# Kernel tuning notes

Measured on AMD Instinct MI355X. Metric: run time of the kernel, lower is better.

## Reference

```python
import jax, jax.numpy as jnp
import numpy as np
import math

B, T, D = 2, 2048, 1024
NH = 16
HD = D // NH


def setup_inputs() -> dict:
    key = jax.random.key(0)
    k1, k2, k3 = jax.random.split(key, 3)
    scale = 0.02
    x = jax.random.normal(k1, (B, T, D), dtype=jnp.float32)
    Wqkv = jax.random.normal(k2, (D, 3 * D), dtype=jnp.float32) * scale
    bqkv = jnp.zeros((3 * D,), dtype=jnp.float32)
    Wproj = jax.random.normal(k3, (D, D), dtype=jnp.float32) * scale
    bproj = jnp.zeros((D,), dtype=jnp.float32)
    return {"x": x, "Wqkv": Wqkv, "bqkv": bqkv, "Wproj": Wproj, "bproj": bproj}


def reference(x, Wqkv, bqkv, Wproj, bproj):
    b, t, c = x.shape
    qkv = x @ Wqkv + bqkv                      # [B,T,3D]
    q, k, v = jnp.split(qkv, 3, axis=2)
    # [B,T,NH,HD] -> [B,NH,T,HD]
    q = q.reshape(b, t, NH, HD).transpose(0, 2, 1, 3)
    k = k.reshape(b, t, NH, HD).transpose(0, 2, 1, 3)
    v = v.reshape(b, t, NH, HD).transpose(0, 2, 1, 3)
    att = jnp.einsum('bhqd,bhkd->bhqk', q, k) / math.sqrt(HD)  # [B,NH,T,T]
    causal = jnp.tril(jnp.ones((t, t), dtype=bool))
    att = jnp.where(causal, att, -jnp.inf)
    att = jax.nn.softmax(att, axis=-1)
    y = jnp.einsum('bhqk,bhkd->bhqd', att, v)  # [B,NH,T,HD]
    y = y.transpose(0, 2, 1, 3).reshape(b, t, c)
    return y @ Wproj + bproj
```

## Files before the change

kernel.cpp:

```cpp
#include <hip/hip_runtime.h>
#include <hip/hip_bf16.h>

#define B_   2
#define T_   2048
#define D_   1024
#define NH_  16
#define HD_  64
#define MROWS (B_*T_)
#define HEADELEMS (B_*NH_*T_*HD_)

#define QSCALE 0.180336880f

typedef unsigned short u16;
typedef unsigned int   u32;

typedef float f32x4  __attribute__((ext_vector_type(4)));
typedef short bf16x8 __attribute__((ext_vector_type(8)));

#define GLP(g, l) __builtin_amdgcn_global_load_lds(                         \
    (const __attribute__((address_space(1))) void*)(g),                     \
    (__attribute__((address_space(3))) void*)(l), 16, 0, 0)

struct Fc { static constexpr bool value = false; };
struct Tc { static constexpr bool value = true;  };

__device__ __forceinline__ u16 f2bf(float f) {
    u32 x = __float_as_uint(f);
    u32 r = (x + 0x7fffu + ((x >> 16) & 1u)) >> 16;
    return (u16)r;
}
__device__ __forceinline__ u32 pkbf2(float a, float b) {
    __hip_bfloat162 h = __float22bfloat162_rn(make_float2(a, b));
    union { __hip_bfloat162 h2; u32 u; } cv; cv.h2 = h; return cv.u;
}

__device__ __forceinline__ void transpose_tile(const float* in, u16* out,
                                               int K, int N, int bx, int by,
                                               int t, float (*Ts)[65])
{
    const int n0 = bx * 64;
    const int k0 = by * 64;
    #pragma unroll
    for (int pass = 0; pass < 4; pass++) {
        const int r = pass * 16 + (t >> 4);
        const int c = (t & 15) * 4;
        float4 v = *(const float4*)(in + (size_t)(k0 + r) * N + n0 + c);
        Ts[r][c] = v.x; Ts[r][c+1] = v.y; Ts[r][c+2] = v.z; Ts[r][c+3] = v.w;
    }
    __syncthreads();
    #pragma unroll
    for (int pass = 0; pass < 2; pass++) {
        const int nn = pass * 32 + (t >> 3);
        const int kk = (t & 7) * 8;
        u16 o[8];
        #pragma unroll
        for (int j = 0; j < 8; j++) o[j] = f2bf(Ts[kk + j][nn]);
        *(uint4*)(out + (size_t)(n0 + nn) * K + k0 + kk) = *(const uint4*)o;
    }
}

__global__ __launch_bounds__(256)
void prep_kernel(const float* __restrict__ x, const float* __restrict__ Wqkv,
                 const float* __restrict__ Wproj, u16* __restrict__ xb,
                 u16* __restrict__ WqkvT, u16* __restrict__ WprojT)
{
    __shared__ float Ts[64][65];
    const int bid = blockIdx.x;
    const int t   = threadIdx.x;
    if (bid < 4096) {
        int i = bid * 256 + t;
        float4 v = ((const float4*)x)[i];
        ushort4 o;
        o.x = f2bf(v.x); o.y = f2bf(v.y); o.z = f2bf(v.z); o.w = f2bf(v.w);
        ((ushort4*)xb)[i] = o;
    } else if (bid < 4096 + 768) {
        int tb = bid - 4096;
        transpose_tile(Wqkv, WqkvT, D_, 3*D_, tb % 48, tb / 48, t, Ts);
    } else {
        int tb = bid - 4864;
        transpose_tile(Wproj, WprojT, D_, D_, tb % 16, tb / 16, t, Ts);
    }
}

__global__ __launch_bounds__(256)
void transpose_conv_kernel(const float* __restrict__ in, u16* __restrict__ out,
                           int K, int N)
{
    __shared__ float Ts[64][65];
    transpose_tile(in, out, K, N, blockIdx.x, blockIdx.y, threadIdx.x, Ts);
}

template <int MODE>
__global__ __launch_bounds__(256)
void gemm_mfma(const u16* __restrict__ A, const u16* __restrict__ BT,
               const float* __restrict__ bias, void* __restrict__ outv,
               int M, int N, int K)
{
    __shared__ u16 As[2][128][64];
    __shared__ u16 Bs[2][128][64];

    const int t    = threadIdx.x;
    const int wave = t >> 6;
    const int lane = t & 63;
    const int l16  = lane & 15;
    const int quad = lane >> 4;

    const int m0 = blockIdx.y * 128;
    const int n0 = blockIdx.x * 128;
    const int mb = (wave >> 1) * 64;
    const int nb = (wave & 1) * 64;

    const int srow = t >> 3;
    const int sseg = ((t & 7) ^ (srow & 7)) * 8;
    const int rw8  = wave * 8;

    const u16* gA = A  + (size_t)(m0 + srow) * K + sseg;
    const u16* gB = BT + (size_t)(n0 + srow) * K + sseg;

    const int fragcol = (quad ^ (l16 & 7)) * 8;

    f32x4 acc[4][4];
    #pragma unroll
    for (int i = 0; i < 4; i++)
        #pragma unroll
        for (int j = 0; j < 4; j++) acc[i][j] = (f32x4){0,0,0,0};

    auto STAGE = [&](int buf, int k0) {
        GLP(gA + k0,          &As[buf][rw8     ][0]);
        GLP(gA + k0 + 32*K,   &As[buf][rw8 + 32][0]);
        GLP(gA + k0 + 64*K,   &As[buf][rw8 + 64][0]);
        GLP(gA + k0 + 96*K,   &As[buf][rw8 + 96][0]);
        GLP(gB + k0,          &Bs[buf][rw8     ][0]);
        GLP(gB + k0 + 32*K,   &Bs[buf][rw8 + 32][0]);
        GLP(gB + k0 + 64*K,   &Bs[buf][rw8 + 64][0]);
        GLP(gB + k0 + 96*K,   &Bs[buf][rw8 + 96][0]);
    };

    const int nk = K >> 6;

    STAGE(0, 0);
    asm volatile("s_waitcnt vmcnt(0)" ::: "memory");
    __builtin_amdgcn_s_barrier();

    for (int kt = 0; kt < nk; ++kt) {
        const int cur = kt & 1;
        const bool have_next = (kt + 1 < nk);

        if (have_next) {
            STAGE(cur ^ 1, (kt + 1) << 6);
            asm volatile("s_waitcnt vmcnt(8)" ::: "memory");
        } else {
            asm volatile("s_waitcnt vmcnt(0)" ::: "memory");
        }
        __builtin_amdgcn_s_barrier();

        #pragma unroll
        for (int kk = 0; kk < 2; kk++) {
            const int fc = fragcol ^ (kk << 5);
            bf16x8 af[4], bfr[4];
            #pragma unroll
            for (int i = 0; i < 4; i++)
                af[i] = *(const bf16x8*)&As[cur][mb + i*16 + l16][fc];
            #pragma unroll
            for (int j = 0; j < 4; j++)
                bfr[j] = *(const bf16x8*)&Bs[cur][nb + j*16 + l16][fc];

            #pragma unroll
            for (int i = 0; i < 4; i++)
                #pragma unroll
                for (int j = 0; j < 4; j++)
                    acc[i][j] = __builtin_amdgcn_mfma_f32_16x16x32_bf16(
                        af[i], bfr[j], acc[i][j], 0, 0, 0);
        }

        if (have_next) {
            asm volatile("s_waitcnt lgkmcnt(0)" ::: "memory");
            __builtin_amdgcn_s_barrier();
        }
    }

    if (MODE == 0) {
        #pragma unroll
        for (int j = 0; j < 4; j++) {
            const int n = n0 + nb + j*16 + l16;
            const float bv = bias[n];
            #pragma unroll
            for (int i = 0; i < 4; i++) {
                #pragma unroll
                for (int r = 0; r < 4; r++) {
                    const int m = m0 + mb + i*16 + quad*4 + r;
                    ((float*)outv)[(size_t)m * N + n] = acc[i][j][r] + bv;
                }
            }
        }
    } else {
        const int sec = n0 >> 10;
        const int b   = m0 >> 11;
        const int tb  = m0 & 2047;
        if (sec < 2) {
            const float qs = (sec == 0) ? QSCALE : 1.f;
            #pragma unroll
            for (int j = 0; j < 4; j++) {
                const int n  = n0 + nb + j*16 + l16;
                const float bv = bias[n];
                const int dd = n & 1023;
                const int h  = dd >> 6;
                const int hd = dd & 63;
                u16* op = (u16*)outv + (size_t)sec * HEADELEMS
                        + ((size_t)(b*NH_ + h)) * T_ * HD_ + hd;
                #pragma unroll
                for (int i = 0; i < 4; i++) {
                    #pragma unroll
                    for (int r = 0; r < 4; r++) {
                        const int tt = tb + mb + i*16 + quad*4 + r;
                        op[(size_t)tt * HD_] = f2bf((acc[i][j][r] + bv) * qs);
                    }
                }
            }
        } else {
            #pragma unroll
            for (int j = 0; j < 4; j++) {
                const int n  = n0 + nb + j*16 + l16;
                const float bv = bias[n];
                const int dd = n & 1023;
                const int h  = dd >> 6;
                const int hd = dd & 63;
                u16* vp = (u16*)outv + (size_t)2 * HEADELEMS
                        + ((size_t)(b*NH_ + h)) * T_ * HD_
                        + (size_t)hd * T_ + tb + mb;
                #pragma unroll
                for (int i = 0; i < 4; i++) {
                    u16 o[4];
                    #pragma unroll
                    for (int r = 0; r < 4; r++) o[r] = f2bf(acc[i][j][r] + bv);
                    *(uint2*)(vp + i*16 + quad*4) = *(const uint2*)o;
                }
            }
        }
    }
}

__global__ __launch_bounds__(256)
void attn_mfma_kernel(const u16* __restrict__ Q, const u16* __restrict__ K,
                      const u16* __restrict__ VT, u16* __restrict__ y1)
{
    __shared__ u16 Ks[2][64][64];
    __shared__ u16 Vs[2][64][64];

    const int t    = threadIdx.x;
    const int wave = t >> 6;
    const int lane = t & 63;
    const int l16  = lane & 15;
    const int quad = lane >> 4;

    const int hb = blockIdx.x;
    const int yy = blockIdx.y;
    const int a  = yy & 7, g = yy >> 3;
    const int qt = (g == 0) ? 31 - a : (g == 1) ? 16 + a
                 : (g == 2) ? 15 - a : a;
    const int b  = hb >> 4;
    const int h  = hb & 15;
    const size_t base = (size_t)hb * T_ * HD_;

    const int qw0 = qt * 64 + wave * 16;

    bf16x8 qf[2];
    {
        const u16* qp = Q + base + (size_t)(qw0 + l16) * HD_ + quad * 8;
        qf[0] = *(const bf16x8*)(qp);
        qf[1] = *(const bf16x8*)(qp + 32);
    }

    bf16x8 onesf;
    #pragma unroll
    for (int i = 0; i < 8; i++) onesf[i] = (short)0x3F80;

    f32x4 o[4];
    #pragma unroll
    for (int d = 0; d < 4; d++) o[d] = (f32x4){0,0,0,0};
    f32x4 accl = (f32x4){0,0,0,0};

    const int nsteps = qt + 1;

    const int srow = t >> 3;
    const int scol = (t & 7) * 8;
    const int sst  = (((t & 7) ^ (srow & 7)) * 8);

    const int fs0 = (quad ^ (l16 & 7)) * 8;
    const int fs1 = fs0 ^ 32;

    const int srcA  = l16 + ((quad & 1) << 5);
    const int srcB  = srcA + 16;
    const bool selhi = (quad >> 1) != 0;

    uint4 kr0, kr1, vr0, vr1;
    {
        const u16* kp = K + base + (size_t)srow * HD_ + scol;
        kr0 = *(const uint4*)kp;
        kr1 = *(const uint4*)(kp + 32 * HD_);
        const u16* vp = VT + base + (size_t)srow * T_ + scol;
        vr0 = *(const uint4*)vp;
        vr1 = *(const uint4*)(vp + 32 * T_);
        *(uint4*)&Ks[0][srow][sst]      = kr0;
        *(uint4*)&Ks[0][srow + 32][sst] = kr1;
        *(uint4*)&Vs[0][srow][sst]      = vr0;
        *(uint4*)&Vs[0][srow + 32][sst] = vr1;
    }
    __syncthreads();

    auto compute_tile = [&](int cur, int k0, auto mc) {
        constexpr bool MASKED = decltype(mc)::value;
        f32x4 st[4];
        __builtin_amdgcn_s_setprio(1);
        #pragma unroll
        for (int j = 0; j < 4; j++) {
            bf16x8 kf0 = *(const bf16x8*)&Ks[cur][j*16 + l16][fs0];
            bf16x8 kf1 = *(const bf16x8*)&Ks[cur][j*16 + l16][fs1];
            f32x4 z = {0,0,0,0};
            z = __builtin_amdgcn_mfma_f32_16x16x32_bf16(kf0, qf[0], z, 0, 0, 0);
            st[j] = __builtin_amdgcn_mfma_f32_16x16x32_bf16(kf1, qf[1], z, 0, 0, 0);
        }
        __builtin_amdgcn_s_setprio(0);

        u32 p01[4], p23[4];
        const int qi = qw0 + l16;
        #pragma unroll
        for (int j = 0; j < 4; j++) {
            const int kb = k0 + j*16 + quad*4;
            float e0 = __builtin_amdgcn_exp2f(st[j][0]);
            float e1 = __builtin_amdgcn_exp2f(st[j][1]);
            float e2 = __builtin_amdgcn_exp2f(st[j][2]);
            float e3 = __builtin_amdgcn_exp2f(st[j][3]);
            if (MASKED) {
                if (kb + 0 > qi) e0 = 0.f;
                if (kb + 1 > qi) e1 = 0.f;
                if (kb + 2 > qi) e2 = 0.f;
                if (kb + 3 > qi) e3 = 0.f;
            }
            p01[j] = pkbf2(e0, e1);
            p23[j] = pkbf2(e2, e3);
        }

        bf16x8 pf[2];
        #pragma unroll
        for (int c = 0; c < 2; c++) {
            u32 t0, t1, r01, r23, r45, r67;
            t0 = (u32)__shfl((int)p01[2*c],   srcA);
            t1 = (u32)__shfl((int)p01[2*c+1], srcA);
            r01 = selhi ? t1 : t0;
            t0 = (u32)__shfl((int)p23[2*c],   srcA);
            t1 = (u32)__shfl((int)p23[2*c+1], srcA);
            r23 = selhi ? t1 : t0;
            t0 = (u32)__shfl((int)p01[2*c],   srcB);
            t1 = (u32)__shfl((int)p01[2*c+1], srcB);
            r45 = selhi ? t1 : t0;
            t0 = (u32)__shfl((int)p23[2*c],   srcB);
            t1 = (u32)__shfl((int)p23[2*c+1], srcB);
            r67 = selhi ? t1 : t0;
            union { u32 u[4]; bf16x8 v; } pk;
            pk.u[0] = r01; pk.u[1] = r23; pk.u[2] = r45; pk.u[3] = r67;
            pf[c] = pk.v;
        }
        __builtin_amdgcn_s_setprio(1);
        accl = __builtin_amdgcn_mfma_f32_16x16x32_bf16(pf[0], onesf, accl, 0, 0, 0);
        accl = __builtin_amdgcn_mfma_f32_16x16x32_bf16(pf[1], onesf, accl, 0, 0, 0);
        #pragma unroll
        for (int d = 0; d < 4; d++) {
            bf16x8 v0 = *(const bf16x8*)&Vs[cur][d*16 + l16][fs0];
            bf16x8 v1 = *(const bf16x8*)&Vs[cur][d*16 + l16][fs1];
            o[d] = __builtin_amdgcn_mfma_f32_16x16x32_bf16(pf[0], v0, o[d], 0, 0, 0);
            o[d] = __builtin_amdgcn_mfma_f32_16x16x32_bf16(pf[1], v1, o[d], 0, 0, 0);
        }
        __builtin_amdgcn_s_setprio(0);
    };

    for (int kt = 0; kt < nsteps; kt++) {
        const int cur = kt & 1;
        const int k0  = kt * 64;
        const bool have_next = (kt + 1 < nsteps);

        if (have_next) {
            const u16* kp = K + base + (size_t)(k0 + 64 + srow) * HD_ + scol;
            kr0 = *(const uint4*)kp;
            kr1 = *(const uint4*)(kp + 32 * HD_);
            const u16* vp = VT + base + (size_t)srow * T_ + k0 + 64 + scol;
            vr0 = *(const uint4*)vp;
            vr1 = *(const uint4*)(vp + 32 * T_);
        }

        if (kt < qt) compute_tile(cur, k0, Fc{});
        else         compute_tile(cur, k0, Tc{});

        if (have_next) {
            const int nxt = cur ^ 1;
            *(uint4*)&Ks[nxt][srow][sst]      = kr0;
            *(uint4*)&Ks[nxt][srow + 32][sst] = kr1;
            *(uint4*)&Vs[nxt][srow][sst]      = vr0;
            *(uint4*)&Vs[nxt][srow + 32][sst] = vr1;
            __syncthreads();
        }
    }

    #pragma unroll
    for (int r = 0; r < 4; r++) {
        const float inv = 1.f / accl[r];
        const int qi = qw0 + quad*4 + r;
        u16* yp = y1 + ((size_t)(b * T_ + qi)) * D_ + h * HD_ + l16;
        yp[0]  = f2bf(o[0][r] * inv);
        yp[16] = f2bf(o[1][r] * inv);
        yp[32] = f2bf(o[2][r] * inv);
        yp[48] = f2bf(o[3][r] * inv);
    }
}

extern "C" void kernel_launch(void* const* d_in, const int* in_sizes, int n_in,
                              void* d_out, int out_size, void* d_ws, size_t ws_size,
                              hipStream_t stream)
{
    const float* x     = (const float*)d_in[0];
    const float* Wqkv  = (const float*)d_in[1];
    const float* bqkv  = (const float*)d_in[2];
    const float* Wproj = (const float*)d_in[3];
    const float* bproj = (const float*)d_in[4];

    u16* scratch = (u16*)d_out;
    u16* xb      = scratch;
    u16* WqkvT   = scratch + (size_t)MROWS * D_;

    const size_t Y1E = (size_t)MROWS * D_;
    const size_t WPE = (size_t)D_ * D_;

    u16* qkv = (u16*)d_ws;
    u16* Qp  = qkv;
    u16* Kp  = qkv + (size_t)HEADELEMS;
    u16* Vtp = qkv + (size_t)2 * HEADELEMS;

    const bool huge = ws_size >= ((size_t)3 * HEADELEMS + Y1E + WPE) * 2;
    const bool big  = ws_size >= ((size_t)3 * HEADELEMS + Y1E) * 2;

    u16* y1b    = big ? qkv + (size_t)3 * HEADELEMS : scratch;
    u16* y1g    = big ? y1b : Vtp;
    u16* WprojT = huge ? qkv + (size_t)3 * HEADELEMS + Y1E : Kp;

    prep_kernel<<<huge ? 5120 : 4864, 256, 0, stream>>>(
        x, Wqkv, Wproj, xb, WqkvT, WprojT);

    gemm_mfma<1><<<dim3(3*D_/128, MROWS/128), 256, 0, stream>>>(
        xb, WqkvT, bqkv, (void*)qkv, MROWS, 3*D_, D_);

    attn_mfma_kernel<<<dim3(NH_*B_, T_/64), 256, 0, stream>>>(Qp, Kp, Vtp, y1b);

    if (!huge)
        transpose_conv_kernel<<<dim3(D_/64, D_/64), 256, 0, stream>>>(
            Wproj, WprojT, D_, D_);

    if (!big)
        (void)hipMemcpyAsync(y1g, y1b, Y1E * sizeof(u16),
                             hipMemcpyDeviceToDevice, stream);

    gemm_mfma<0><<<dim3(D_/128, MROWS/128), 256, 0, stream>>>(
        y1g, WprojT, bproj, d_out, MROWS, D_, D_);
}
```

Before: 190.1 us.

## Pair complementary causal query tiles per attention block to share K/V loads

Each attention block now processes two query tiles, p and 31-p, instead of one. Every block therefore does the same amount of causal work, and each K/V tile staged in LDS serves both query tiles for the first p+1 steps. The grid is halved to 512 blocks. Each thread now keeps two sets of accumulators, which raises register pressure and may lower occupancy, and fewer blocks means less parallelism on the GPU.

```diff
diff --git a/kernel.cpp b/kernel.cpp
--- a/kernel.cpp
+++ b/kernel.cpp
@@ -254,33 +254,37 @@
     const int quad = lane >> 4;
 
     const int hb = blockIdx.x;
-    const int yy = blockIdx.y;
-    const int a  = yy & 7, g = yy >> 3;
-    const int qt = (g == 0) ? 31 - a : (g == 1) ? 16 + a
-                 : (g == 2) ? 15 - a : a;
+    const int p  = blockIdx.y;
+    const int qta = p;
+    const int qtb = 31 - p;
     const int b  = hb >> 4;
     const int h  = hb & 15;
     const size_t base = (size_t)hb * T_ * HD_;
 
-    const int qw0 = qt * 64 + wave * 16;
-
-    bf16x8 qf[2];
+    const int qwA = qta * 64 + wave * 16;
+    const int qwB = qtb * 64 + wave * 16;
+
+    bf16x8 qfA[2], qfB[2];
     {
-        const u16* qp = Q + base + (size_t)(qw0 + l16) * HD_ + quad * 8;
-        qf[0] = *(const bf16x8*)(qp);
-        qf[1] = *(const bf16x8*)(qp + 32);
+        const u16* qa = Q + base + (size_t)(qwA + l16) * HD_ + quad * 8;
+        qfA[0] = *(const bf16x8*)(qa);
+        qfA[1] = *(const bf16x8*)(qa + 32);
+        const u16* qb = Q + base + (size_t)(qwB + l16) * HD_ + quad * 8;
+        qfB[0] = *(const bf16x8*)(qb);
+        qfB[1] = *(const bf16x8*)(qb + 32);
     }
 
     bf16x8 onesf;
     #pragma unroll
     for (int i = 0; i < 8; i++) onesf[i] = (short)0x3F80;
 
-    f32x4 o[4];
-    #pragma unroll
-    for (int d = 0; d < 4; d++) o[d] = (f32x4){0,0,0,0};
-    f32x4 accl = (f32x4){0,0,0,0};
-
-    const int nsteps = qt + 1;
+    f32x4 oA[4], oB[4];
+    #pragma unroll
+    for (int d = 0; d < 4; d++) { oA[d] = (f32x4){0,0,0,0}; oB[d] = (f32x4){0,0,0,0}; }
+    f32x4 acclA = (f32x4){0,0,0,0};
+    f32x4 acclB = (f32x4){0,0,0,0};
+
+    const int nsteps = qtb + 1;
 
     const int srow = t >> 3;
     const int scol = (t & 7) * 8;
@@ -308,7 +312,8 @@
     }
     __syncthreads();
 
-    auto compute_tile = [&](int cur, int k0, auto mc) {
+    auto compute_tile = [&](int cur, int k0, auto mc, const bf16x8* qf,
+                            f32x4* o, f32x4& accl, int qw0) {
         constexpr bool MASKED = decltype(mc)::value;
         f32x4 st[4];
         __builtin_amdgcn_s_setprio(1);
@@ -388,8 +393,17 @@
             vr1 = *(const uint4*)(vp + 32 * T_);
         }
 
-        if (kt < qt) compute_tile(cur, k0, Fc{});
-        else         compute_tile(cur, k0, Tc{});
+        if (kt < qta) {
+            compute_tile(cur, k0, Fc{}, qfA, oA, acclA, qwA);
+            compute_tile(cur, k0, Fc{}, qfB, oB, acclB, qwB);
+        } else if (kt == qta) {
+            compute_tile(cur, k0, Tc{}, qfA, oA, acclA, qwA);
+            compute_tile(cur, k0, Fc{}, qfB, oB, acclB, qwB);
+        } else if (kt < qtb) {
+            compute_tile(cur, k0, Fc{}, qfB, oB, acclB, qwB);
+        } else {
+            compute_tile(cur, k0, Tc{}, qfB, oB, acclB, qwB);
+        }
 
         if (have_next) {
             const int nxt = cur ^ 1;
@@ -403,13 +417,21 @@
 
     #pragma unroll
     for (int r = 0; r < 4; r++) {
-        const float inv = 1.f / accl[r];
-        const int qi = qw0 + quad*4 + r;
-        u16* yp = y1 + ((size_t)(b * T_ + qi)) * D_ + h * HD_ + l16;
-        yp[0]  = f2bf(o[0][r] * inv);
-        yp[16] = f2bf(o[1][r] * inv);
-        yp[32] = f2bf(o[2][r] * inv);
-        yp[48] = f2bf(o[3][r] * inv);
+        const float invA = 1.f / acclA[r];
+        const int qiA = qwA + quad*4 + r;
+        u16* ya = y1 + ((size_t)(b * T_ + qiA)) * D_ + h * HD_ + l16;
+        ya[0]  = f2bf(oA[0][r] * invA);
+        ya[16] = f2bf(oA[1][r] * invA);
+        ya[32] = f2bf(oA[2][r] * invA);
+        ya[48] = f2bf(oA[3][r] * invA);
+
+        const float invB = 1.f / acclB[r];
+        const int qiB = qwB + quad*4 + r;
+        u16* yb = y1 + ((size_t)(b * T_ + qiB)) * D_ + h * HD_ + l16;
+        yb[0]  = f2bf(oB[0][r] * invB);
+        yb[16] = f2bf(oB[1][r] * invB);
+        yb[32] = f2bf(oB[2][r] * invB);
+        yb[48] = f2bf(oB[3][r] * invB);
     }
 }
 
@@ -448,7 +470,7 @@
     gemm_mfma<1><<<dim3(3*D_/128, MROWS/128), 256, 0, stream>>>(
         xb, WqkvT, bqkv, (void*)qkv, MROWS, 3*D_, D_);
 
-    attn_mfma_kernel<<<dim3(NH_*B_, T_/64), 256, 0, stream>>>(Qp, Kp, Vtp, y1b);
+    attn_mfma_kernel<<<dim3(NH_*B_, 16), 256, 0, stream>>>(Qp, Kp, Vtp, y1b);
 
     if (!huge)
         transpose_conv_kernel<<<dim3(D_/64, D_/64), 256, 0, stream>>>(
```

New measurement: 194.5 us. 2.3% more time.

## Stage attention K/V tiles via global_load_lds direct-to-LDS async copies

Applied to the files above, without the earlier changes.

Replaces the register-staged double-buffered K/V tile loads in the attention kernel with global_load_lds direct copies into LDS. The XOR swizzle moves from the LDS write address to the global read address. Explicit vmcnt/lgkmcnt waits and raw s_barrier calls replace __syncthreads. This is meant to free VGPRs and remove the LDS store instructions so that loads overlap better with MFMA work. The gain depends on the manual waitcnt accounting being correct, and the swizzled global addressing may reduce coalescing.

```diff
diff --git a/kernel.cpp b/kernel.cpp
--- a/kernel.cpp
+++ b/kernel.cpp
@@ -283,8 +283,11 @@
     const int nsteps = qt + 1;
 
     const int srow = t >> 3;
-    const int scol = (t & 7) * 8;
-    const int sst  = (((t & 7) ^ (srow & 7)) * 8);
+    const int sseg = ((t & 7) ^ (srow & 7)) * 8;
+    const int rw8  = wave * 8;
+
+    const u16* gK = K  + base + (size_t)srow * HD_ + sseg;
+    const u16* gV = VT + base + (size_t)srow * T_  + sseg;
 
     const int fs0 = (quad ^ (l16 & 7)) * 8;
     const int fs1 = fs0 ^ 32;
@@ -293,20 +296,12 @@
     const int srcB  = srcA + 16;
     const bool selhi = (quad >> 1) != 0;
 
-    uint4 kr0, kr1, vr0, vr1;
-    {
-        const u16* kp = K + base + (size_t)srow * HD_ + scol;
-        kr0 = *(const uint4*)kp;
-        kr1 = *(const uint4*)(kp + 32 * HD_);
-        const u16* vp = VT + base + (size_t)srow * T_ + scol;
-        vr0 = *(const uint4*)vp;
-        vr1 = *(const uint4*)(vp + 32 * T_);
-        *(uint4*)&Ks[0][srow][sst]      = kr0;
-        *(uint4*)&Ks[0][srow + 32][sst] = kr1;
-        *(uint4*)&Vs[0][srow][sst]      = vr0;
-        *(uint4*)&Vs[0][srow + 32][sst] = vr1;
-    }
-    __syncthreads();
+    auto STAGE = [&](int buf, int k0) {
+        GLP(gK + (size_t)(k0     ) * HD_, &Ks[buf][rw8     ][0]);
+        GLP(gK + (size_t)(k0 + 32) * HD_, &Ks[buf][rw8 + 32][0]);
+        GLP(gV + k0,                      &Vs[buf][rw8     ][0]);
+        GLP(gV + k0 + 32 * T_,            &Vs[buf][rw8 + 32][0]);
+    };
 
     auto compute_tile = [&](int cur, int k0, auto mc) {
         constexpr bool MASKED = decltype(mc)::value;
@@ -374,30 +369,29 @@
         __builtin_amdgcn_s_setprio(0);
     };
 
+    STAGE(0, 0);
+    asm volatile("s_waitcnt vmcnt(0)" ::: "memory");
+    __builtin_amdgcn_s_barrier();
+
     for (int kt = 0; kt < nsteps; kt++) {
         const int cur = kt & 1;
         const int k0  = kt * 64;
         const bool have_next = (kt + 1 < nsteps);
 
         if (have_next) {
-            const u16* kp = K + base + (size_t)(k0 + 64 + srow) * HD_ + scol;
-            kr0 = *(const uint4*)kp;
-            kr1 = *(const uint4*)(kp + 32 * HD_);
-            const u16* vp = VT + base + (size_t)srow * T_ + k0 + 64 + scol;
-            vr0 = *(const uint4*)vp;
-            vr1 = *(const uint4*)(vp + 32 * T_);
-        }
+            STAGE(cur ^ 1, k0 + 64);
+            asm volatile("s_waitcnt vmcnt(4)" ::: "memory");
+        } else {
+            asm volatile("s_waitcnt vmcnt(0)" ::: "memory");
+        }
+        __builtin_amdgcn_s_barrier();
 
         if (kt < qt) compute_tile(cur, k0, Fc{});
         else         compute_tile(cur, k0, Tc{});
 
         if (have_next) {
-            const int nxt = cur ^ 1;
-            *(uint4*)&Ks[nxt][srow][sst]      = kr0;
-            *(uint4*)&Ks[nxt][srow + 32][sst] = kr1;
-            *(uint4*)&Vs[nxt][srow][sst]      = vr0;
-            *(uint4*)&Vs[nxt][srow + 32][sst] = vr1;
-            __syncthreads();
+            asm volatile("s_waitcnt lgkmcnt(0)" ::: "memory");
+            __builtin_amdgcn_s_barrier();
         }
     }
 
```

Measured after the change: 191.5 us. Within noise of the previous version (+0.7%).
